# Kernel tuning notes

Measured on AMD Instinct MI355X. Metric: run time of the kernel, lower is better.

## Reference

```python
import jax, jax.numpy as jnp
import numpy as np

K, PMAX, NUM_PTS = 20000, 30, 5
GEO_DIM, PE_DIM = 256, 32
C_OUT = GEO_DIM - PE_DIM  # 224
NUM_FREQS = 8


def setup_inputs() -> dict:
    key = jax.random.key(0)
    k = jax.random.split(key, 6)
    geoms = jax.random.normal(k[0], (K, PMAX, 2), dtype=jnp.float32) * 8.0  # ego BEV meters
    lengths = jax.random.randint(k[1], (K,), 2, PMAX + 1)                   # valid points per polyline
    w1 = jax.random.normal(k[2], (C_OUT // 2, 2, 3), jnp.float32) * 0.2
    b1 = jax.random.normal(k[3], (C_OUT // 2,), jnp.float32) * 0.02
    w2 = jax.random.normal(k[4], (C_OUT, C_OUT // 2, 3), jnp.float32) * 0.05
    b2 = jax.random.normal(k[5], (C_OUT,), jnp.float32) * 0.02
    gamma = jnp.ones((C_OUT,), jnp.float32)
    beta = jnp.zeros((C_OUT,), jnp.float32)
    return {"geoms": geoms, "lengths": lengths, "w1": w1, "b1": b1,
            "w2": w2, "b2": b2, "gamma": gamma, "beta": beta,
            "roi_w": 60, "roi_h": 30}


def _resample_one(coords, L):
    # coords: [PMAX,2] padded polyline; L: scalar int (>=2 valid points)
    diffs = coords[1:] - coords[:-1]                                  # [PMAX-1,2]
    sq = jnp.sum(diffs * diffs, axis=1)
    mask = (jnp.arange(PMAX - 1) < (L - 1)).astype(coords.dtype)      # valid segments
    seg = jnp.where(sq > 0, jnp.sqrt(jnp.where(sq > 0, sq, 1.0)), 0.0) * mask
    cum = jnp.concatenate([jnp.zeros((1,), coords.dtype), jnp.cumsum(seg)])  # [PMAX]
    total = cum[-1]
    targets = jnp.linspace(0.0, 1.0, NUM_PTS, dtype=coords.dtype) * total
    idx = jnp.clip(jnp.searchsorted(cum, targets, side='left'), 1, L - 1)
    t = (targets - cum[idx - 1]) / (seg[idx - 1] + 1e-8)
    pts = coords[idx - 1] + t[:, None] * diffs[idx - 1]               # [NUM_PTS,2]
    degen = total < 1e-6
    return jnp.where(degen, jnp.broadcast_to(coords[0], pts.shape), pts)


def _conv1d(x, w, b):
    # x: [K,C,5]; w: [O,C,3]; 'same' padding 1
    y = jax.lax.conv_general_dilated(x, w, (1,), ((1, 1),),
                                     dimension_numbers=('NCH', 'OIH', 'NCH'))
    return y + b[None, :, None]


def reference(geoms, lengths, w1, b1, w2, b2, gamma, beta, roi_w, roi_h):
    resampled = jax.vmap(_resample_one)(geoms, lengths)               # [K,5,2]
    roi_half = jnp.array([roi_w / 2.0, roi_h / 2.0], jnp.float32)
    roi_full = jnp.array([float(roi_w), float(roi_h)], jnp.float32)
    coords = (resampled + roi_half) / roi_full                        # [K,5,2] in [0,1]
    # sinusoidal PE: per coord dim [sin(x*2^f*pi) x8 | cos x8] -> flatten to 32
    freqs = (2.0 ** jnp.arange(NUM_FREQS, dtype=jnp.float32)) * np.float32(np.pi)
    xf = coords[..., None] * freqs                                    # [K,5,2,8]
    pe = jnp.concatenate([jnp.sin(xf), jnp.cos(xf)], axis=-1).reshape(-1, NUM_PTS, PE_DIM)
    x = coords.transpose(0, 2, 1)                                     # [K,2,5]
    x = jax.nn.relu(_conv1d(x, w1, b1))                               # [K,112,5]
    x = jax.nn.relu(_conv1d(x, w2, b2))                               # [K,224,5]
    x = x.transpose(0, 2, 1)                                          # [K,5,224]
    mu = jnp.mean(x, axis=-1, keepdims=True)
    var = jnp.mean((x - mu) ** 2, axis=-1, keepdims=True)
    x = (x - mu) * jax.lax.rsqrt(var + 1e-5) * gamma + beta
    geo_feats = jnp.concatenate([pe, x], axis=-1)                     # [K,5,256]
    return geo_feats, coords
```

## Files before the change

### kernel.cpp

```cpp
#include <hip/hip_runtime.h>
#include <math.h>

#define K_POLY   20000
#define PMAX     30
#define NUM_PTS  5
#define C_MID    112
#define C_OUT    224
#define PE_DIM   32
#define GEO_DIM  256
#define M_ROWS   (K_POLY*NUM_PTS)

#define NTILES   14
#define KSTEPS   11
#define WP_ELEMS (KSTEPS*NTILES*64*8)
#define NPACK_BLK ((WP_ELEMS+255)/256)
#define POLY_PER_BLK 4
#define NPREP_BLK ((K_POLY+POLY_PER_BLK-1)/POLY_PER_BLK)

#define GROUP_US 8192

#define ROWS_W   32
#define NUNITS   (M_ROWS/ROWS_W)
#define WAVES2_B 12
#define NBLK2    256
#define TOTW2    (NBLK2*WAVES2_B)

typedef __attribute__((ext_vector_type(8))) short short8;
typedef __attribute__((ext_vector_type(4))) float f32x4;

__device__ inline unsigned short f2bf(float f) {
    union { float f; unsigned u; } v; v.f = f;
    return (unsigned short)((v.u + 0x7fffu + ((v.u >> 16) & 1u)) >> 16);
}

#define GLDS(gp, lp) __builtin_amdgcn_global_load_lds( \
    (const __attribute__((address_space(1))) void*)(gp), \
    (__attribute__((address_space(3))) void*)(lp), 16, 0, 0)

__device__ inline void store_frag(unsigned short* Af, int r, int k, unsigned short v) {
    size_t addr = (size_t)(r >> 4) * GROUP_US + (size_t)(k >> 5) * 512
                + (size_t)(((((k >> 3) & 3) << 4) + (r & 15)) << 3) + (k & 7);
    Af[addr] = v;
}

__global__ __launch_bounds__(256) void prep_pack(
    const float* __restrict__ geoms, const int* __restrict__ lengths,
    const float* __restrict__ w1, const float* __restrict__ b1,
    const float* __restrict__ w2,
    const int* __restrict__ roi_w, const int* __restrict__ roi_h,
    unsigned short* __restrict__ Wp, float* __restrict__ out)
{
    if (blockIdx.x < NPACK_BLK) {
        int i = blockIdx.x * 256 + threadIdx.x;
        if (i < WP_ELEMS) {
            int j    = i & 7;
            int lane = (i >> 3) & 63;
            int grp  = i >> 9;
            int nt   = grp % NTILES;
            int ks   = grp / NTILES;
            int k    = ks * 32 + (lane >> 4) * 8 + j;
            int n    = nt * 16 + (lane & 15);
            float v = 0.f;
            if (k < 336) {
                int dk = k / C_MID, c = k - dk * C_MID;
                v = w2[(n * C_MID + c) * 3 + dk];
            }
            Wp[i] = f2bf(v);
        }
        return;
    }

    const int poly = (blockIdx.x - NPACK_BLK) * POLY_PER_BLK + (threadIdx.x >> 6);
    const int lane = threadIdx.x & 63;
    if (poly >= K_POLY) return;

    const float* gp = geoms + (size_t)poly * (PMAX * 2);
    float px = 0.f, py = 0.f;
    if (lane < PMAX) { float2 p = ((const float2*)gp)[lane]; px = p.x; py = p.y; }
    const int L = lengths[poly];

    float nx = __shfl(px, lane + 1);
    float ny = __shfl(py, lane + 1);
    float seg = 0.f;
    if (lane < L - 1 && lane < PMAX - 1) {
        float dx = nx - px, dy = ny - py;
        float sq = dx * dx + dy * dy;
        seg = (sq > 0.f) ? sqrtf(sq) : 0.f;
    }
    float incl = seg;
    #pragma unroll
    for (int d = 1; d < 32; d <<= 1) {
        float v = __shfl_up(incl, d, 32);
        if ((lane & 31) >= d) incl += v;
    }
    float cum = __shfl_up(incl, 1, 32);
    if ((lane & 31) == 0) cum = 0.f;
    const float total = __shfl(incl, PMAX - 2);

    const float roiw = (float)roi_w[0], roih = (float)roi_h[0];
    const float halfx = roiw * 0.5f, halfy = roih * 0.5f;
    const bool degen = total < 1e-6f;
    const float x0g = __shfl(px, 0), y0g = __shfl(py, 0);

    float bxv[NUM_PTS], byv[NUM_PTS];
    #pragma unroll
    for (int j = 0; j < NUM_PTS; ++j) {
        float tj = total * (0.25f * (float)j);
        unsigned long long mlt = __ballot(lane < PMAX && cum < tj);
        int idx = (int)__popcll(mlt);
        idx = max(1, min(idx, L - 1));
        float c1 = __shfl(cum, idx - 1);
        float s1 = __shfl(seg, idx - 1);
        float ax = __shfl(px, idx - 1), ay = __shfl(py, idx - 1);
        float bx2 = __shfl(px, idx),    by2 = __shfl(py, idx);
        float tt = (tj - c1) / (s1 + 1e-8f);
        float fx = degen ? x0g : ax + tt * (bx2 - ax);
        float fy = degen ? y0g : ay + tt * (by2 - ay);
        bxv[j] = (fx + halfx) / roiw;
        byv[j] = (fy + halfy) / roih;
    }
    if (lane == 0) {
        float* co = out + (size_t)M_ROWS * GEO_DIM + (size_t)poly * (NUM_PTS * 2);
        #pragma unroll
        for (int j = 0; j < NUM_PTS; ++j) { co[2 * j] = bxv[j]; co[2 * j + 1] = byv[j]; }
    }

    unsigned short* Af = (unsigned short*)out;
    const int rbase = poly * NUM_PTS;

    for (int z = lane; z < 80; z += 64)
        store_frag(Af, rbase + (z >> 4), 336 + (z & 15), 0);

    #pragma unroll
    for (int it = 0; it < 2; ++it) {
        int c = it * 64 + lane;
        if (c < C_MID) {
            const float* w = w1 + c * 6;
            float w0 = w[0], wa = w[1], wb = w[2], w3 = w[3], w4 = w[4], w5 = w[5];
            float bb = b1[c];
            store_frag(Af, rbase + 0, c, 0);
            store_frag(Af, rbase + 4, 224 + c, 0);
            #pragma unroll
            for (int pp = 0; pp < NUM_PTS; ++pp) {
                float acc = bb + bxv[pp] * wa + byv[pp] * w4;
                if (pp > 0)           acc += bxv[pp - 1] * w0 + byv[pp - 1] * w3;
                if (pp < NUM_PTS - 1) acc += bxv[pp + 1] * wb + byv[pp + 1] * w5;
                unsigned short hv = f2bf(fmaxf(acc, 0.f));
                #pragma unroll
                for (int dk = 0; dk < 3; ++dk) {
                    int p = pp + 1 - dk;
                    if (p >= 0 && p < NUM_PTS)
                        store_frag(Af, rbase + p, dk * C_MID + c, hv);
                }
            }
        }
    }
}

__global__ __launch_bounds__(768, 3) void gemm2(
    const unsigned short* __restrict__ Wp,
    const float* __restrict__ b2, const float* __restrict__ gamma,
    const float* __restrict__ beta, float* __restrict__ out)
{
    __shared__ __align__(16) unsigned short s_B[WP_ELEMS];
    __shared__ float s_ln[3 * C_OUT];

    const int t = threadIdx.x, lane = t & 63, wave = t >> 6;
    const int quad = lane >> 4, m = lane & 15;

    #pragma unroll
    for (int it = 0; it < 13; ++it) {
        int idx = t + it * 768;
        if (idx < WP_ELEMS / 8)
            GLDS((const char*)Wp + (size_t)idx * 16, (char*)s_B + idx * 16);
    }
    if (t < C_OUT) {
        s_ln[t]             = b2[t];
        s_ln[C_OUT + t]     = gamma[t];
        s_ln[2 * C_OUT + t] = beta[t];
    }
    __syncthreads();

    const unsigned short* Af = (const unsigned short*)out;
    const float* cptr = out + (size_t)M_ROWS * GEO_DIM;
    const unsigned short* bl = s_B + lane * 8;

    for (int u = blockIdx.x * WAVES2_B + wave; u < NUNITS; u += TOTW2) {
        const int rw = u * ROWS_W;

        const unsigned short* Ab0 = Af + (size_t)(2 * u) * GROUP_US + lane * 8;
        const unsigned short* Ab1 = Ab0 + GROUP_US;

        float cv = cptr[(size_t)rw * 2 + lane];

        f32x4 acc0[NTILES], acc1[NTILES];
        #pragma unroll
        for (int nt = 0; nt < NTILES; ++nt)
            #pragma unroll
            for (int i = 0; i < 4; ++i) { acc0[nt][i] = 0.f; acc1[nt][i] = 0.f; }

        short8 a0 = *(const short8*)Ab0;
        short8 a1 = *(const short8*)Ab1;
        #pragma unroll
        for (int ks = 0; ks < KSTEPS; ++ks) {
            short8 a0n = a0, a1n = a1;
            if (ks < KSTEPS - 1) {
                a0n = *(const short8*)(Ab0 + (ks + 1) * 512);
                a1n = *(const short8*)(Ab1 + (ks + 1) * 512);
            }
            const unsigned short* bp = bl + ks * (NTILES * 512);
            __builtin_amdgcn_s_setprio(1);
            #pragma unroll
            for (int nt = 0; nt < NTILES; ++nt) {
                short8 b = *(const short8*)(bp + nt * 512);
                acc0[nt] = __builtin_amdgcn_mfma_f32_16x16x32_bf16(a0, b, acc0[nt], 0, 0, 0);
                acc1[nt] = __builtin_amdgcn_mfma_f32_16x16x32_bf16(a1, b, acc1[nt], 0, 0, 0);
            }
            __builtin_amdgcn_s_setprio(0);
            a0 = a0n; a1 = a1n;
        }

        {
            const int col = lane & 31;
            const int d = col >> 4, isc = (col >> 3) & 1, fr = col & 7;
            const float pef = (float)(1 << fr) * 3.14159265358979323846f;
            #pragma unroll
            for (int it = 0; it < 16; ++it) {
                int j2 = it * 2 + (lane >> 5);
                float x = __shfl(cv, j2 * 2 + d);
                float arg = x * pef;
                out[(size_t)(rw + j2) * GEO_DIM + col] = isc ? __cosf(arg) : __sinf(arg);
            }
        }

        unsigned lnoff = 0;
        asm volatile("" : "+v"(lnoff));
        float bias[NTILES], gm[NTILES], bt[NTILES];
        #pragma unroll
        for (int nt = 0; nt < NTILES; ++nt) {
            unsigned col = lnoff + nt * 16 + m;
            bias[nt] = s_ln[col];
            gm[nt]   = s_ln[C_OUT + col];
            bt[nt]   = s_ln[2 * C_OUT + col];
        }

        #pragma unroll
        for (int g = 0; g < 2; ++g) {
            f32x4* acc = g ? acc1 : acc0;
            #pragma unroll
            for (int i = 0; i < 4; ++i) {
                float s = 0.f, q = 0.f;
                #pragma unroll
                for (int nt = 0; nt < NTILES; ++nt) {
                    float v = fmaxf(acc[nt][i] + bias[nt], 0.f);
                    acc[nt][i] = v;
                    s += v; q += v * v;
                }
                #pragma unroll
                for (int mk = 8; mk >= 1; mk >>= 1) {
                    s += __shfl_xor(s, mk, 64);
                    q += __shfl_xor(q, mk, 64);
                }
                float mu  = s * (1.f / C_OUT);
                float var = fmaxf(q * (1.f / C_OUT) - mu * mu, 0.f);
                float rs  = rsqrtf(var + 1e-5f);
                int r = rw + g * 16 + quad * 4 + i;
                size_t ob = (size_t)r * GEO_DIM + PE_DIM + m;
                #pragma unroll
                for (int nt = 0; nt < NTILES; ++nt)
                    out[ob + nt * 16] = (acc[nt][i] - mu) * rs * gm[nt] + bt[nt];
            }
        }
    }
}

extern "C" void kernel_launch(void* const* d_in, const int* in_sizes, int n_in,
                              void* d_out, int out_size, void* d_ws, size_t ws_size,
                              hipStream_t stream) {
    const float* geoms   = (const float*)d_in[0];
    const int*   lengths = (const int*)d_in[1];
    const float* w1      = (const float*)d_in[2];
    const float* b1      = (const float*)d_in[3];
    const float* w2      = (const float*)d_in[4];
    const float* b2      = (const float*)d_in[5];
    const float* gamma   = (const float*)d_in[6];
    const float* beta    = (const float*)d_in[7];
    const int*   roi_w   = (const int*)d_in[8];
    const int*   roi_h   = (const int*)d_in[9];
    float* out = (float*)d_out;
    unsigned short* Wp = (unsigned short*)d_ws;

    hipLaunchKernelGGL(prep_pack, dim3(NPACK_BLK + NPREP_BLK), dim3(256), 0, stream,
                       geoms, lengths, w1, b1, w2, roi_w, roi_h, Wp, out);
    hipLaunchKernelGGL(gemm2, dim3(NBLK2), dim3(768), 0, stream, Wp, b2, gamma, beta, out);
}
```

Before: 193.2 us.

## Stage conv1 activations in LDS and write A fragments with vector stores

```diff
diff --git a/kernel.cpp b/kernel.cpp
--- a/kernel.cpp
+++ b/kernel.cpp
@@ -14,14 +14,13 @@
 #define KSTEPS   11
 #define WP_ELEMS (KSTEPS*NTILES*64*8)
 #define NPACK_BLK ((WP_ELEMS+255)/256)
-#define POLY_PER_BLK 4
-#define NPREP_BLK ((K_POLY+POLY_PER_BLK-1)/POLY_PER_BLK)
 
 #define GROUP_US 8192
 
 #define ROWS_W   32
 #define NUNITS   (M_ROWS/ROWS_W)
-#define WAVES2_B 12
+#define NPREP_BLK NUNITS
+#define WAVES2_B 8
 #define NBLK2    256
 #define TOTW2    (NBLK2*WAVES2_B)
 
@@ -37,11 +36,7 @@
     (const __attribute__((address_space(1))) void*)(gp), \
     (__attribute__((address_space(3))) void*)(lp), 16, 0, 0)
 
-__device__ inline void store_frag(unsigned short* Af, int r, int k, unsigned short v) {
-    size_t addr = (size_t)(r >> 4) * GROUP_US + (size_t)(k >> 5) * 512
-                + (size_t)(((((k >> 3) & 3) << 4) + (r & 15)) << 3) + (k & 7);
-    Af[addr] = v;
-}
+#define SH_PITCH 120
 
 __global__ __launch_bounds__(256) void prep_pack(
     const float* __restrict__ geoms, const int* __restrict__ lengths,
@@ -50,6 +45,8 @@
     const int* __restrict__ roi_w, const int* __restrict__ roi_h,
     unsigned short* __restrict__ Wp, float* __restrict__ out)
 {
+    __shared__ unsigned short s_h[40 * SH_PITCH];
+
     if (blockIdx.x < NPACK_BLK) {
         int i = blockIdx.x * 256 + threadIdx.x;
         if (i < WP_ELEMS) {
@@ -70,114 +67,126 @@
         return;
     }
 
-    const int poly = (blockIdx.x - NPACK_BLK) * POLY_PER_BLK + (threadIdx.x >> 6);
-    const int lane = threadIdx.x & 63;
-    if (poly >= K_POLY) return;
-
-    const float* gp = geoms + (size_t)poly * (PMAX * 2);
-    float px = 0.f, py = 0.f;
-    if (lane < PMAX) { float2 p = ((const float2*)gp)[lane]; px = p.x; py = p.y; }
-    const int L = lengths[poly];
-
-    float nx = __shfl(px, lane + 1);
-    float ny = __shfl(py, lane + 1);
-    float seg = 0.f;
-    if (lane < L - 1 && lane < PMAX - 1) {
-        float dx = nx - px, dy = ny - py;
-        float sq = dx * dx + dy * dy;
-        seg = (sq > 0.f) ? sqrtf(sq) : 0.f;
-    }
-    float incl = seg;
-    #pragma unroll
-    for (int d = 1; d < 32; d <<= 1) {
-        float v = __shfl_up(incl, d, 32);
-        if ((lane & 31) >= d) incl += v;
-    }
-    float cum = __shfl_up(incl, 1, 32);
-    if ((lane & 31) == 0) cum = 0.f;
-    const float total = __shfl(incl, PMAX - 2);
-
-    const float roiw = (float)roi_w[0], roih = (float)roi_h[0];
+    const int ub     = blockIdx.x - NPACK_BLK;
+    const int rbase0 = ub * ROWS_W;
+    const int pstart = rbase0 / 5;
+    const int npoly  = (rbase0 + 31) / 5 - pstart + 1;
+
+    const int t = threadIdx.x, lane = t & 63, wave = t >> 6;
+    const float roiw  = (float)roi_w[0], roih = (float)roi_h[0];
     const float halfx = roiw * 0.5f, halfy = roih * 0.5f;
-    const bool degen = total < 1e-6f;
-    const float x0g = __shfl(px, 0), y0g = __shfl(py, 0);
-
-    float bxv[NUM_PTS], byv[NUM_PTS];
-    #pragma unroll
-    for (int j = 0; j < NUM_PTS; ++j) {
-        float tj = total * (0.25f * (float)j);
-        unsigned long long mlt = __ballot(lane < PMAX && cum < tj);
-        int idx = (int)__popcll(mlt);
-        idx = max(1, min(idx, L - 1));
-        float c1 = __shfl(cum, idx - 1);
-        float s1 = __shfl(seg, idx - 1);
-        float ax = __shfl(px, idx - 1), ay = __shfl(py, idx - 1);
-        float bx2 = __shfl(px, idx),    by2 = __shfl(py, idx);
-        float tt = (tj - c1) / (s1 + 1e-8f);
-        float fx = degen ? x0g : ax + tt * (bx2 - ax);
-        float fy = degen ? y0g : ay + tt * (by2 - ay);
-        bxv[j] = (fx + halfx) / roiw;
-        byv[j] = (fy + halfy) / roih;
-    }
-    if (lane == 0) {
-        float* co = out + (size_t)M_ROWS * GEO_DIM + (size_t)poly * (NUM_PTS * 2);
-        #pragma unroll
-        for (int j = 0; j < NUM_PTS; ++j) { co[2 * j] = bxv[j]; co[2 * j + 1] = byv[j]; }
-    }
+
+    for (int lp = wave; lp < 8; lp += 4) {
+        if (lp < npoly) {
+            const int poly = pstart + lp;
+            const float* gp = geoms + (size_t)poly * (PMAX * 2);
+            float px = 0.f, py = 0.f;
+            if (lane < PMAX) { float2 p = ((const float2*)gp)[lane]; px = p.x; py = p.y; }
+            const int L = lengths[poly];
+
+            float nx = __shfl(px, lane + 1);
+            float ny = __shfl(py, lane + 1);
+            float seg = 0.f;
+            if (lane < L - 1 && lane < PMAX - 1) {
+                float dx = nx - px, dy = ny - py;
+                float sq = dx * dx + dy * dy;
+                seg = (sq > 0.f) ? sqrtf(sq) : 0.f;
+            }
+            float incl = seg;
+            #pragma unroll
+            for (int d = 1; d < 32; d <<= 1) {
+                float v = __shfl_up(incl, d, 32);
+                if ((lane & 31) >= d) incl += v;
+            }
+            float cum = __shfl_up(incl, 1, 32);
+            if ((lane & 31) == 0) cum = 0.f;
+            const float total = __shfl(incl, PMAX - 2);
+            const bool degen = total < 1e-6f;
+            const float x0g = __shfl(px, 0), y0g = __shfl(py, 0);
+
+            float bxv[NUM_PTS], byv[NUM_PTS];
+            #pragma unroll
+            for (int j = 0; j < NUM_PTS; ++j) {
+                float tj = total * (0.25f * (float)j);
+                unsigned long long mlt = __ballot(lane < PMAX && cum < tj);
+                int idx = (int)__popcll(mlt);
+                idx = max(1, min(idx, L - 1));
+                float c1 = __shfl(cum, idx - 1);
+                float s1 = __shfl(seg, idx - 1);
+                float ax = __shfl(px, idx - 1), ay = __shfl(py, idx - 1);
+                float bx2 = __shfl(px, idx),    by2 = __shfl(py, idx);
+                float tt = (tj - c1) / (s1 + 1e-8f);
+                float fx = degen ? x0g : ax + tt * (bx2 - ax);
+                float fy = degen ? y0g : ay + tt * (by2 - ay);
+                bxv[j] = (fx + halfx) / roiw;
+                byv[j] = (fy + halfy) / roih;
+            }
+            if (lane == 0) {
+                float* co = out + (size_t)M_ROWS * GEO_DIM + (size_t)poly * (NUM_PTS * 2);
+                #pragma unroll
+                for (int j = 0; j < NUM_PTS; ++j) { co[2 * j] = bxv[j]; co[2 * j + 1] = byv[j]; }
+            }
+
+            #pragma unroll
+            for (int it = 0; it < 2; ++it) {
+                int c = it * 64 + lane;
+                if (c < C_MID) {
+                    const float* w = w1 + c * 6;
+                    float w0 = w[0], wa = w[1], wb = w[2], w3 = w[3], w4 = w[4], w5 = w[5];
+                    float bb = b1[c];
+                    #pragma unroll
+                    for (int pp = 0; pp < NUM_PTS; ++pp) {
+                        float acc = bb + bxv[pp] * wa + byv[pp] * w4;
+                        if (pp > 0)           acc += bxv[pp - 1] * w0 + byv[pp - 1] * w3;
+                        if (pp < NUM_PTS - 1) acc += bxv[pp + 1] * wb + byv[pp + 1] * w5;
+                        s_h[(lp * 5 + pp) * SH_PITCH + c] = f2bf(fmaxf(acc, 0.f));
+                    }
+                }
+            }
+        }
+    }
+    __syncthreads();
 
     unsigned short* Af = (unsigned short*)out;
-    const int rbase = poly * NUM_PTS;
-
-    for (int z = lane; z < 80; z += 64)
-        store_frag(Af, rbase + (z >> 4), 336 + (z & 15), 0);
-
-    #pragma unroll
-    for (int it = 0; it < 2; ++it) {
-        int c = it * 64 + lane;
-        if (c < C_MID) {
-            const float* w = w1 + c * 6;
-            float w0 = w[0], wa = w[1], wb = w[2], w3 = w[3], w4 = w[4], w5 = w[5];
-            float bb = b1[c];
-            store_frag(Af, rbase + 0, c, 0);
-            store_frag(Af, rbase + 4, 224 + c, 0);
-            #pragma unroll
-            for (int pp = 0; pp < NUM_PTS; ++pp) {
-                float acc = bb + bxv[pp] * wa + byv[pp] * w4;
-                if (pp > 0)           acc += bxv[pp - 1] * w0 + byv[pp - 1] * w3;
-                if (pp < NUM_PTS - 1) acc += bxv[pp + 1] * wb + byv[pp + 1] * w5;
-                unsigned short hv = f2bf(fmaxf(acc, 0.f));
-                #pragma unroll
-                for (int dk = 0; dk < 3; ++dk) {
-                    int p = pp + 1 - dk;
-                    if (p >= 0 && p < NUM_PTS)
-                        store_frag(Af, rbase + p, dk * C_MID + c, hv);
-                }
-            }
-        }
+    for (int cidx = t; cidx < 2 * KSTEPS * 64; cidx += 256) {
+        int gl  = cidx / (KSTEPS * 64);
+        int rem = cidx - gl * (KSTEPS * 64);
+        int ks  = rem >> 6;
+        int ln  = rem & 63;
+        int q   = ln >> 4, rr = ln & 15;
+        int r   = (2 * ub + gl) * 16 + rr;
+        int p   = r % 5;
+        int lp5 = (r - pstart * 5) - p;
+
+        union { short8 v; unsigned long long u2[2]; } val;
+        val.u2[0] = 0ull; val.u2[1] = 0ull;
+        int k0 = ks * 32 + q * 8;
+        if (k0 < 336) {
+            int dk = k0 / C_MID;
+            int c0 = k0 - dk * C_MID;
+            int pp = p + dk - 1;
+            if (pp >= 0 && pp < NUM_PTS)
+                val.v = *(const short8*)&s_h[(lp5 + pp) * SH_PITCH + c0];
+        }
+        *(short8*)(Af + (size_t)(2 * ub + gl) * GROUP_US + ks * 512 + ln * 8) = val.v;
     }
 }
 
-__global__ __launch_bounds__(768, 3) void gemm2(
+__global__ __launch_bounds__(512, 2) void gemm2(
     const unsigned short* __restrict__ Wp,
     const float* __restrict__ b2, const float* __restrict__ gamma,
     const float* __restrict__ beta, float* __restrict__ out)
 {
     __shared__ __align__(16) unsigned short s_B[WP_ELEMS];
-    __shared__ float s_ln[3 * C_OUT];
 
     const int t = threadIdx.x, lane = t & 63, wave = t >> 6;
     const int quad = lane >> 4, m = lane & 15;
 
     #pragma unroll
-    for (int it = 0; it < 13; ++it) {
-        int idx = t + it * 768;
+    for (int it = 0; it < 20; ++it) {
+        int idx = t + it * 512;
         if (idx < WP_ELEMS / 8)
             GLDS((const char*)Wp + (size_t)idx * 16, (char*)s_B + idx * 16);
-    }
-    if (t < C_OUT) {
-        s_ln[t]             = b2[t];
-        s_ln[C_OUT + t]     = gamma[t];
-        s_ln[2 * C_OUT + t] = beta[t];
     }
     __syncthreads();
 
@@ -233,15 +242,11 @@
             }
         }
 
-        unsigned lnoff = 0;
-        asm volatile("" : "+v"(lnoff));
         float bias[NTILES], gm[NTILES], bt[NTILES];
         #pragma unroll
         for (int nt = 0; nt < NTILES; ++nt) {
-            unsigned col = lnoff + nt * 16 + m;
-            bias[nt] = s_ln[col];
-            gm[nt]   = s_ln[C_OUT + col];
-            bt[nt]   = s_ln[2 * C_OUT + col];
+            int col = nt * 16 + m;
+            bias[nt] = b2[col]; gm[nt] = gamma[col]; bt[nt] = beta[col];
         }
 
         #pragma unroll
@@ -292,5 +297,5 @@
 
     hipLaunchKernelGGL(prep_pack, dim3(NPACK_BLK + NPREP_BLK), dim3(256), 0, stream,
                        geoms, lengths, w1, b1, w2, roi_w, roi_h, Wp, out);
-    hipLaunchKernelGGL(gemm2, dim3(NBLK2), dim3(768), 0, stream, Wp, b2, gamma, beta, out);
+    hipLaunchKernelGGL(gemm2, dim3(NBLK2), dim3(512), 0, stream, Wp, b2, gamma, beta, out);
 }
```

Result: faster. 175.8 us (-9.0%).
